# Kernel tuning notes

Measured on AMD Instinct MI355X. Metric: run time of the kernel, lower is better.

The kernel has to match this reference:

```python
import jax, jax.numpy as jnp
import numpy as np

SEQ, BATCH, EMB = 2048, 8, 1024
HEADS, PROJ = 8, 64


def setup_inputs() -> dict:
    key = jax.random.key(0)
    ks = jax.random.split(key, 7)
    x = jax.random.normal(ks[0], (SEQ, BATCH, EMB), dtype=jnp.float32)
    # pz.nn.Linear: pure einsum weight, no bias
    w_in = jax.random.normal(ks[1], (EMB, HEADS, PROJ), dtype=jnp.float32) / np.sqrt(EMB)
    # eqx.nn.GRUCell params: weight_ih (3P, P_in), weight_hh (3P, P), bias (3P,), bias_n (P,)
    w_ih = jax.random.normal(ks[2], (3 * PROJ, PROJ), dtype=jnp.float32) / np.sqrt(PROJ)
    w_hh = jax.random.normal(ks[3], (3 * PROJ, PROJ), dtype=jnp.float32) / np.sqrt(PROJ)
    b_ih = jax.random.normal(ks[4], (3 * PROJ,), dtype=jnp.float32) * 0.01
    b_n = jax.random.normal(ks[5], (PROJ,), dtype=jnp.float32) * 0.01
    w_out = jax.random.normal(ks[6], (HEADS, PROJ, EMB), dtype=jnp.float32) / np.sqrt(HEADS * PROJ)
    return {"x": x, "w_in": w_in, "w_ih": w_ih, "w_hh": w_hh, "b_ih": b_ih, "b_n": b_n, "w_out": w_out}


def reference(x, w_in, w_ih, w_hh, b_ih, b_n, w_out):
    # project_from_embedding: [S,B,E] -> [S,B,H,P]
    xp = jnp.einsum("sbe,ehp->sbhp", x, w_in)

    def step(h, xt):
        # xt, h: [B,H,P]; GRU cell shared across batch and heads
        ig = jnp.einsum("bhp,gp->bhg", xt, w_ih) + b_ih  # [B,H,3P]
        hg = jnp.einsum("bhp,gp->bhg", h, w_hh)
        ir, iz, inn = jnp.split(ig, 3, axis=-1)
        hr, hz, hn = jnp.split(hg, 3, axis=-1)
        r = jax.nn.sigmoid(ir + hr)
        z = jax.nn.sigmoid(iz + hz)
        n = jnp.tanh(inn + r * (hn + b_n))
        h_new = n + z * (h - n)
        return h_new, h_new

    h0 = jnp.zeros((BATCH, HEADS, PROJ), dtype=x.dtype)
    _, ys = jax.lax.scan(step, h0, xp)  # ys: [S,B,H,P]
    # project_to_embedding: [S,B,H,P] -> [S,B,E]
    return jnp.einsum("sbhp,hpe->sbe", ys, w_out)
```

## Files before the change

### kernel.cpp

```cpp
#include <hip/hip_runtime.h>
#include <math.h>

#define SEQ    2048
#define BATCH  8
#define EMB    1024
#define HEADS  8
#define PROJ   64
#define CHAINS 64
#define GATES  192

#define SRZ (-1.4426950408889634f)
#define SN  ( 2.8853900817779268f)

typedef float f4  __attribute__((ext_vector_type(4)));
typedef short s8v __attribute__((ext_vector_type(8)));
typedef _Float16 h2v __attribute__((ext_vector_type(2)));

static __device__ __forceinline__ float bf2f(unsigned short u) {
    union { unsigned int i; float f; } c; c.i = ((unsigned int)u) << 16; return c.f;
}
static __device__ __forceinline__ unsigned short f2bf(float f) {
    union { float f; unsigned int i; } c; c.f = f;
    unsigned int u = c.i;
    u += 0x7fffu + ((u >> 16) & 1u);
    return (unsigned short)(u >> 16);
}
static __device__ __forceinline__ float fdot2u(unsigned int a, unsigned int b, float c) {
    union { unsigned int u; h2v h; } ua, ub; ua.u = a; ub.u = b;
    return __builtin_amdgcn_fdot2(ua.h, ub.h, c, false);
}

__global__ __launch_bounds__(256)
void transpose_to_bf16(const float* __restrict__ in, unsigned short* __restrict__ out,
                       int R, int C) {
    __shared__ float tile[32][33];
    const int tx = threadIdx.x & 31, ty = threadIdx.x >> 5;
    const int c0 = blockIdx.x * 32, r0 = blockIdx.y * 32;
#pragma unroll
    for (int i = 0; i < 4; ++i)
        tile[ty + i * 8][tx] = in[(size_t)(r0 + ty + i * 8) * C + c0 + tx];
    __syncthreads();
#pragma unroll
    for (int i = 0; i < 4; ++i)
        out[(size_t)(c0 + ty + i * 8) * R + r0 + tx] = f2bf(tile[tx][ty + i * 8]);
}

__global__ void convert_wih_scaled(const float* __restrict__ in, unsigned short* __restrict__ out) {
    const int i = blockIdx.x * blockDim.x + threadIdx.x;
    if (i < GATES * PROJ) {
        const float s = (i < 128 * PROJ) ? SRZ : SN;
        out[i] = f2bf(in[i] * s);
    }
}

__global__ void convert_whh_scaled(const float* __restrict__ in, unsigned short* __restrict__ out) {
    const int i = blockIdx.x * blockDim.x + threadIdx.x;
    if (i < GATES * PROJ) {
        const float s = (i < 128 * PROJ) ? SRZ : SN;
        union { _Float16 h; unsigned short u; } c;
        c.h = (_Float16)(in[i] * s);
        out[i] = c.u;
    }
}

__global__ void scale_bias(const float* __restrict__ in, float* __restrict__ out) {
    const int i = threadIdx.x;
    if (i < GATES) out[i] = in[i] * ((i < 128) ? SRZ : SN);
}

template <int BM, int BN, int BK, bool A_F32, typename OutT, bool BIAS, bool PERM>
__global__ __launch_bounds__((BM / 64) * (BN / 64) * 64)
void gemm_mfma(const void* __restrict__ Ap, const unsigned short* __restrict__ BT,
               OutT* __restrict__ C, const float* __restrict__ bias,
               int M, int N, int K) {
    constexpr int NWN = BN / 64;
    constexpr int NW  = (BM / 64) * NWN;
    constexpr int NT  = NW * 64;
    constexpr int KP  = BK + 8;
    __shared__ unsigned short Al[BM * KP];
    __shared__ unsigned short Bl[BN * KP];

    const int t    = threadIdx.x, lane = t & 63, wid = t >> 6;
    const int wm   = (wid / NWN) * 64, wn = (wid % NWN) * 64;
    const int bm   = blockIdx.x * BM, bn = blockIdx.y * BN;
    const int fr   = lane & 15;
    const int fq   = lane >> 4;

    f4 acc[4][4];
#pragma unroll
    for (int m = 0; m < 4; ++m)
#pragma unroll
        for (int n = 0; n < 4; ++n) acc[m][n] = f4{0.f, 0.f, 0.f, 0.f};

    const int nkt = K / BK;
    for (int kt = 0; kt < nkt; ++kt) {
        const int k0 = kt * BK;
        __syncthreads();
        constexpr int CHA = (BM * BK / 8) / NT;
#pragma unroll
        for (int i = 0; i < CHA; ++i) {
            const int ci = t + i * NT;
            const int r = ci / (BK / 8), cc = (ci % (BK / 8)) * 8;
            if constexpr (A_F32) {
                const float* A = (const float*)Ap;
                const float4 u0 = *(const float4*)&A[(size_t)(bm + r) * K + k0 + cc];
                const float4 u1 = *(const float4*)&A[(size_t)(bm + r) * K + k0 + cc + 4];
                s8v w;
                w[0] = (short)f2bf(u0.x); w[1] = (short)f2bf(u0.y);
                w[2] = (short)f2bf(u0.z); w[3] = (short)f2bf(u0.w);
                w[4] = (short)f2bf(u1.x); w[5] = (short)f2bf(u1.y);
                w[6] = (short)f2bf(u1.z); w[7] = (short)f2bf(u1.w);
                *(s8v*)&Al[r * KP + cc] = w;
            } else {
                const unsigned short* A = (const unsigned short*)Ap;
                *(s8v*)&Al[r * KP + cc] = *(const s8v*)&A[(size_t)(bm + r) * K + k0 + cc];
            }
        }
        constexpr int CHB = (BN * BK / 8) / NT;
#pragma unroll
        for (int i = 0; i < CHB; ++i) {
            const int ci = t + i * NT;
            const int r = ci / (BK / 8), cc = (ci % (BK / 8)) * 8;
            *(s8v*)&Bl[r * KP + cc] = *(const s8v*)&BT[(size_t)(bn + r) * K + k0 + cc];
        }
        __syncthreads();
#pragma unroll
        for (int ks = 0; ks < BK / 32; ++ks) {
            s8v av[4], bv[4];
#pragma unroll
            for (int m = 0; m < 4; ++m)
                av[m] = *(const s8v*)&Al[(wm + m * 16 + fr) * KP + ks * 32 + fq * 8];
#pragma unroll
            for (int n = 0; n < 4; ++n)
                bv[n] = *(const s8v*)&Bl[(wn + n * 16 + fr) * KP + ks * 32 + fq * 8];
#pragma unroll
            for (int m = 0; m < 4; ++m)
#pragma unroll
                for (int n = 0; n < 4; ++n)
                    acc[m][n] = __builtin_amdgcn_mfma_f32_16x16x32_bf16(
                        av[m], bv[n], acc[m][n], 0, 0, 0);
        }
    }

#pragma unroll
    for (int n = 0; n < 4; ++n) {
        const int col = bn + wn + n * 16 + fr;
        const float bv = BIAS ? bias[col] : 0.f;
#pragma unroll
        for (int m = 0; m < 4; ++m) {
            const int row0 = bm + wm + m * 16 + fq * 4;
#pragma unroll
            for (int j = 0; j < 4; ++j) {
                const float val = acc[m][n][j] + bv;
                const int row = row0 + j;
                const size_t orow = PERM ? ((size_t)(row & 63) * SEQ + (row >> 6))
                                         : (size_t)row;
                if constexpr (sizeof(OutT) == 4)
                    C[orow * N + col] = val;
                else
                    C[orow * N + col] = f2bf(val);
            }
        }
    }
}

__global__ __launch_bounds__(64, 1)
void gru_scan8(const unsigned short* __restrict__ w_hh16, const float* __restrict__ b_n,
               const unsigned short* __restrict__ ig, unsigned short* __restrict__ ys) {
    const int c = blockIdx.x;
    const int p = threadIdx.x;

    __shared__ unsigned short hl16[PROJ];

    unsigned int wru[32], wzu[32], wnu[32];
#pragma unroll
    for (int q = 0; q < 8; ++q) {
        const uint4 a = *(const uint4*)&w_hh16[(size_t)(0 * PROJ + p) * PROJ + q * 8];
        wru[4*q+0] = a.x; wru[4*q+1] = a.y; wru[4*q+2] = a.z; wru[4*q+3] = a.w;
        const uint4 b = *(const uint4*)&w_hh16[(size_t)(1 * PROJ + p) * PROJ + q * 8];
        wzu[4*q+0] = b.x; wzu[4*q+1] = b.y; wzu[4*q+2] = b.z; wzu[4*q+3] = b.w;
        const uint4 e = *(const uint4*)&w_hh16[(size_t)(2 * PROJ + p) * PROJ + q * 8];
        wnu[4*q+0] = e.x; wnu[4*q+1] = e.y; wnu[4*q+2] = e.z; wnu[4*q+3] = e.w;
    }
    const float bn2 = b_n[p] * SN;

    float hreg = 0.f;
    unsigned int hw[32];
#pragma unroll
    for (int k = 0; k < 32; ++k) hw[k] = 0u;

    const unsigned short* igc = ig + (size_t)c * SEQ * GATES + p;

    unsigned short pr[4], pz[4], pn[4];
#pragma unroll
    for (int k = 0; k < 4; ++k) {
        const unsigned short* g = igc + (size_t)k * GATES;
        pr[k] = g[0]; pz[k] = g[PROJ]; pn[k] = g[2 * PROJ];
    }

#pragma unroll 4
    for (int s = 0; s < SEQ; ++s) {
        const int u = s & 3;
        const float tr = bf2f(pr[u]);
        const float tz = bf2f(pz[u]);
        const float tn = bf2f(pn[u]);
        {
            int sn = s + 4; if (sn > SEQ - 1) sn = SEQ - 1;
            const unsigned short* g = igc + (size_t)sn * GATES;
            pr[u] = g[0]; pz[u] = g[PROJ]; pn[u] = g[2 * PROJ];
        }

        float ar[4] = {0.f, 0.f, 0.f, 0.f};
#pragma unroll
        for (int k = 0; k < 32; ++k) ar[k & 3] = fdot2u(hw[k], wru[k], ar[k & 3]);
        const float hgr = (ar[0] + ar[1]) + (ar[2] + ar[3]);

        float an[4] = {0.f, 0.f, 0.f, 0.f};
#pragma unroll
        for (int k = 0; k < 32; ++k) an[k & 3] = fdot2u(hw[k], wnu[k], an[k & 3]);
        const float hgn = (an[0] + an[1]) + (an[2] + an[3]);

        float az[4] = {0.f, 0.f, 0.f, 0.f};
#pragma unroll
        for (int k = 0; k < 32; ++k) az[k & 3] = fdot2u(hw[k], wzu[k], az[k & 3]);
        const float hgz = (az[0] + az[1]) + (az[2] + az[3]);

        const float r  = __builtin_amdgcn_rcpf(1.f + __builtin_amdgcn_exp2f(tr + hgr));
        const float z  = __builtin_amdgcn_rcpf(1.f + __builtin_amdgcn_exp2f(tz + hgz));
        const float y2 = fmaf(r, hgn + bn2, tn);
        const float nn = fmaf(-2.f, __builtin_amdgcn_rcpf(1.f + __builtin_amdgcn_exp2f(y2)), 1.f);
        const float hnew = nn + z * (hreg - nn);
        hreg = hnew;

        union { _Float16 h; unsigned short u; } cv; cv.h = (_Float16)hnew;
        hl16[p] = cv.u;
#pragma unroll
        for (int q = 0; q < 8; ++q) {
            const uint4 v = ((const uint4*)hl16)[q];
            hw[4*q+0] = v.x; hw[4*q+1] = v.y; hw[4*q+2] = v.z; hw[4*q+3] = v.w;
        }
        ys[((size_t)s * CHAINS + c) * PROJ + p] = f2bf(hnew);
    }
}

extern "C" void kernel_launch(void* const* d_in, const int* in_sizes, int n_in,
                              void* d_out, int out_size, void* d_ws, size_t ws_size,
                              hipStream_t stream) {
    const float* x     = (const float*)d_in[0];
    const float* w_in  = (const float*)d_in[1];
    const float* w_ih  = (const float*)d_in[2];
    const float* w_hh  = (const float*)d_in[3];
    const float* b_ih  = (const float*)d_in[4];
    const float* b_n   = (const float*)d_in[5];
    const float* w_out = (const float*)d_in[6];
    float* out = (float*)d_out;

    char* ws = (char*)d_ws;
    const size_t xp_bytes  = (size_t)SEQ * CHAINS * PROJ * 2;
    const size_t ig_bytes  = (size_t)SEQ * CHAINS * GATES * 2;
    unsigned short* xp_bf  = (unsigned short*)(ws);
    unsigned short* ysb    = (unsigned short*)(ws);
    unsigned short* ig     = (unsigned short*)(ws + xp_bytes);
    unsigned short* w_inT  = (unsigned short*)(ws + xp_bytes + ig_bytes);
    unsigned short* w_outT = w_inT + (size_t)512 * 1024;
    unsigned short* w_ihb  = w_outT + (size_t)1024 * 512;
    unsigned short* w_hh16 = w_ihb + (size_t)GATES * PROJ;
    float*          bs     = (float*)(w_hh16 + (size_t)GATES * PROJ);

    transpose_to_bf16<<<dim3(512 / 32, 1024 / 32), 256, 0, stream>>>(w_in, w_inT, 1024, 512);
    transpose_to_bf16<<<dim3(1024 / 32, 512 / 32), 256, 0, stream>>>(w_out, w_outT, 512, 1024);
    convert_wih_scaled<<<(GATES * PROJ + 255) / 256, 256, 0, stream>>>(w_ih, w_ihb);
    convert_whh_scaled<<<(GATES * PROJ + 255) / 256, 256, 0, stream>>>(w_hh, w_hh16);
    scale_bias<<<1, 256, 0, stream>>>(b_ih, bs);

    gemm_mfma<128, 128, 64, true, unsigned short, false, false>
        <<<dim3(16384 / 128, 512 / 128), 256, 0, stream>>>(
            x, w_inT, xp_bf, nullptr, 16384, 512, 1024);

    gemm_mfma<128, 64, 64, false, unsigned short, true, true>
        <<<dim3(131072 / 128, 192 / 64), 128, 0, stream>>>(
            xp_bf, w_ihb, ig, bs, 131072, 192, 64);

    gru_scan8<<<CHAINS, 64, 0, stream>>>(w_hh16, b_n, ig, ysb);

    gemm_mfma<128, 128, 64, false, float, false, false>
        <<<dim3(16384 / 128, 1024 / 128), 256, 0, stream>>>(
            ysb, w_outT, out, nullptr, 16384, 1024, 512);
}
```

Before: 734.5 us.

## Interleave two GRU chains per wavefront in the sequential scan

Each scan block now carries two independent recurrence chains, interleaving their per-step dot products, activations and LDS state exchanges, and the launch uses half as many blocks. The aim is to hide the serial dependency latency of one chain (LDS round trip, transcendental ops) behind the other chain's work, at the cost of doubling per-thread work per step and using fewer CUs. Register pressure rises with a second hidden-state vector and a second set of prefetch buffers.

Result: slower. 1.331 ms (+81.3%).

```diff
diff --git a/kernel.cpp b/kernel.cpp
--- a/kernel.cpp
+++ b/kernel.cpp
@@ -165,12 +165,14 @@
 }
 
 __global__ __launch_bounds__(64, 1)
-void gru_scan8(const unsigned short* __restrict__ w_hh16, const float* __restrict__ b_n,
-               const unsigned short* __restrict__ ig, unsigned short* __restrict__ ys) {
-    const int c = blockIdx.x;
+void gru_scan12(const unsigned short* __restrict__ w_hh16, const float* __restrict__ b_n,
+                const unsigned short* __restrict__ ig, unsigned short* __restrict__ ys) {
+    const int blk = blockIdx.x;
+    const int cA = 2 * blk, cB = 2 * blk + 1;
     const int p = threadIdx.x;
 
-    __shared__ unsigned short hl16[PROJ];
+    __shared__ unsigned short hA16[PROJ];
+    __shared__ unsigned short hB16[PROJ];
 
     unsigned int wru[32], wzu[32], wnu[32];
 #pragma unroll
@@ -184,62 +186,114 @@
     }
     const float bn2 = b_n[p] * SN;
 
-    float hreg = 0.f;
-    unsigned int hw[32];
-#pragma unroll
-    for (int k = 0; k < 32; ++k) hw[k] = 0u;
-
-    const unsigned short* igc = ig + (size_t)c * SEQ * GATES + p;
-
-    unsigned short pr[4], pz[4], pn[4];
+    float hregA = 0.f, hregB = 0.f;
+    unsigned int hwA[32], hwB[32];
+#pragma unroll
+    for (int k = 0; k < 32; ++k) { hwA[k] = 0u; hwB[k] = 0u; }
+    hA16[p] = 0; hB16[p] = 0;
+
+    const unsigned short* igcA = ig + (size_t)cA * SEQ * GATES + p;
+    const unsigned short* igcB = ig + (size_t)cB * SEQ * GATES + p;
+
+    unsigned short prA[4], pzA[4], pnA[4], prB[4], pzB[4], pnB[4];
 #pragma unroll
     for (int k = 0; k < 4; ++k) {
-        const unsigned short* g = igc + (size_t)k * GATES;
-        pr[k] = g[0]; pz[k] = g[PROJ]; pn[k] = g[2 * PROJ];
+        const unsigned short* gA = igcA + (size_t)k * GATES;
+        prA[k] = gA[0]; pzA[k] = gA[PROJ]; pnA[k] = gA[2 * PROJ];
+        const unsigned short* gB = igcB + (size_t)k * GATES;
+        prB[k] = gB[0]; pzB[k] = gB[PROJ]; pnB[k] = gB[2 * PROJ];
     }
 
 #pragma unroll 4
     for (int s = 0; s < SEQ; ++s) {
         const int u = s & 3;
-        const float tr = bf2f(pr[u]);
-        const float tz = bf2f(pz[u]);
-        const float tn = bf2f(pn[u]);
+        const int sn4 = (s + 4 > SEQ - 1) ? SEQ - 1 : s + 4;
+
         {
-            int sn = s + 4; if (sn > SEQ - 1) sn = SEQ - 1;
-            const unsigned short* g = igc + (size_t)sn * GATES;
-            pr[u] = g[0]; pz[u] = g[PROJ]; pn[u] = g[2 * PROJ];
-        }
-
-        float ar[4] = {0.f, 0.f, 0.f, 0.f};
-#pragma unroll
-        for (int k = 0; k < 32; ++k) ar[k & 3] = fdot2u(hw[k], wru[k], ar[k & 3]);
-        const float hgr = (ar[0] + ar[1]) + (ar[2] + ar[3]);
-
-        float an[4] = {0.f, 0.f, 0.f, 0.f};
-#pragma unroll
-        for (int k = 0; k < 32; ++k) an[k & 3] = fdot2u(hw[k], wnu[k], an[k & 3]);
-        const float hgn = (an[0] + an[1]) + (an[2] + an[3]);
-
-        float az[4] = {0.f, 0.f, 0.f, 0.f};
-#pragma unroll
-        for (int k = 0; k < 32; ++k) az[k & 3] = fdot2u(hw[k], wzu[k], az[k & 3]);
-        const float hgz = (az[0] + az[1]) + (az[2] + az[3]);
-
-        const float r  = __builtin_amdgcn_rcpf(1.f + __builtin_amdgcn_exp2f(tr + hgr));
-        const float z  = __builtin_amdgcn_rcpf(1.f + __builtin_amdgcn_exp2f(tz + hgz));
-        const float y2 = fmaf(r, hgn + bn2, tn);
-        const float nn = fmaf(-2.f, __builtin_amdgcn_rcpf(1.f + __builtin_amdgcn_exp2f(y2)), 1.f);
-        const float hnew = nn + z * (hreg - nn);
-        hreg = hnew;
-
-        union { _Float16 h; unsigned short u; } cv; cv.h = (_Float16)hnew;
-        hl16[p] = cv.u;
-#pragma unroll
-        for (int q = 0; q < 8; ++q) {
-            const uint4 v = ((const uint4*)hl16)[q];
-            hw[4*q+0] = v.x; hw[4*q+1] = v.y; hw[4*q+2] = v.z; hw[4*q+3] = v.w;
-        }
-        ys[((size_t)s * CHAINS + c) * PROJ + p] = f2bf(hnew);
+            const float tr = bf2f(prA[u]);
+            const float tz = bf2f(pzA[u]);
+            const float tn = bf2f(pnA[u]);
+            {
+                const unsigned short* g = igcA + (size_t)sn4 * GATES;
+                prA[u] = g[0]; pzA[u] = g[PROJ]; pnA[u] = g[2 * PROJ];
+            }
+
+            float ar[4] = {0.f, 0.f, 0.f, 0.f};
+#pragma unroll
+            for (int k = 0; k < 32; ++k) ar[k & 3] = fdot2u(hwA[k], wru[k], ar[k & 3]);
+            const float hgr = (ar[0] + ar[1]) + (ar[2] + ar[3]);
+            const float er  = __builtin_amdgcn_exp2f(tr + hgr);
+
+            float an[4] = {0.f, 0.f, 0.f, 0.f};
+#pragma unroll
+            for (int k = 0; k < 32; ++k) an[k & 3] = fdot2u(hwA[k], wnu[k], an[k & 3]);
+            const float hgn = (an[0] + an[1]) + (an[2] + an[3]);
+
+            float az[4] = {0.f, 0.f, 0.f, 0.f};
+#pragma unroll
+            for (int k = 0; k < 32; ++k) az[k & 3] = fdot2u(hwA[k], wzu[k], az[k & 3]);
+            const float hgz = (az[0] + az[1]) + (az[2] + az[3]);
+            const float ez  = __builtin_amdgcn_exp2f(tz + hgz);
+
+            const float r  = __builtin_amdgcn_rcpf(1.f + er);
+            const float z  = __builtin_amdgcn_rcpf(1.f + ez);
+            const float y2 = fmaf(r, hgn + bn2, tn);
+            const float nn = fmaf(-2.f, __builtin_amdgcn_rcpf(1.f + __builtin_amdgcn_exp2f(y2)), 1.f);
+            const float hnew = nn + z * (hregA - nn);
+            hregA = hnew;
+
+            union { _Float16 h; unsigned short uu; } cv; cv.h = (_Float16)hnew;
+            hA16[p] = cv.uu;
+            ys[((size_t)s * CHAINS + cA) * PROJ + p] = f2bf(hnew);
+#pragma unroll
+            for (int q = 0; q < 8; ++q) {
+                const uint4 v = ((const uint4*)hA16)[q];
+                hwA[4*q+0] = v.x; hwA[4*q+1] = v.y; hwA[4*q+2] = v.z; hwA[4*q+3] = v.w;
+            }
+        }
+
+        {
+            const float tr = bf2f(prB[u]);
+            const float tz = bf2f(pzB[u]);
+            const float tn = bf2f(pnB[u]);
+            {
+                const unsigned short* g = igcB + (size_t)sn4 * GATES;
+                prB[u] = g[0]; pzB[u] = g[PROJ]; pnB[u] = g[2 * PROJ];
+            }
+
+            float ar[4] = {0.f, 0.f, 0.f, 0.f};
+#pragma unroll
+            for (int k = 0; k < 32; ++k) ar[k & 3] = fdot2u(hwB[k], wru[k], ar[k & 3]);
+            const float hgr = (ar[0] + ar[1]) + (ar[2] + ar[3]);
+            const float er  = __builtin_amdgcn_exp2f(tr + hgr);
+
+            float an[4] = {0.f, 0.f, 0.f, 0.f};
+#pragma unroll
+            for (int k = 0; k < 32; ++k) an[k & 3] = fdot2u(hwB[k], wnu[k], an[k & 3]);
+            const float hgn = (an[0] + an[1]) + (an[2] + an[3]);
+
+            float az[4] = {0.f, 0.f, 0.f, 0.f};
+#pragma unroll
+            for (int k = 0; k < 32; ++k) az[k & 3] = fdot2u(hwB[k], wzu[k], az[k & 3]);
+            const float hgz = (az[0] + az[1]) + (az[2] + az[3]);
+            const float ez  = __builtin_amdgcn_exp2f(tz + hgz);
+
+            const float r  = __builtin_amdgcn_rcpf(1.f + er);
+            const float z  = __builtin_amdgcn_rcpf(1.f + ez);
+            const float y2 = fmaf(r, hgn + bn2, tn);
+            const float nn = fmaf(-2.f, __builtin_amdgcn_rcpf(1.f + __builtin_amdgcn_exp2f(y2)), 1.f);
+            const float hnew = nn + z * (hregB - nn);
+            hregB = hnew;
+
+            union { _Float16 h; unsigned short uu; } cv; cv.h = (_Float16)hnew;
+            hB16[p] = cv.uu;
+            ys[((size_t)s * CHAINS + cB) * PROJ + p] = f2bf(hnew);
+#pragma unroll
+            for (int q = 0; q < 8; ++q) {
+                const uint4 v = ((const uint4*)hB16)[q];
+                hwB[4*q+0] = v.x; hwB[4*q+1] = v.y; hwB[4*q+2] = v.z; hwB[4*q+3] = v.w;
+            }
+        }
     }
 }
 
@@ -281,7 +335,7 @@
         <<<dim3(131072 / 128, 192 / 64), 128, 0, stream>>>(
             xp_bf, w_ihb, ig, bs, 131072, 192, 64);
 
-    gru_scan8<<<CHAINS, 64, 0, stream>>>(w_hh16, b_n, ig, ysb);
+    gru_scan12<<<CHAINS / 2, 64, 0, stream>>>(w_hh16, b_n, ig, ysb);
 
     gemm_mfma<128, 128, 64, false, float, false, false>
         <<<dim3(16384 / 128, 1024 / 128), 256, 0, stream>>>(
```
